# Kernel tuning notes

Hardware: AMD Instinct MI355X
Metric: run time of the kernel (lower is better)

Reference implementation:

```python
import jax, jax.numpy as jnp
import numpy as np

N_ITER = 50  # bisection iterations (matches entmax_bisect default)


def entmax_bisect(x, alpha):
    """alpha-entmax via bisection along axis=1. x: [B, L, 1], alpha: [1] (>1)."""
    a_m1 = alpha - 1.0
    inv = 1.0 / a_m1
    xs = x * a_m1
    d = x.shape[1]
    max_val = jnp.max(xs, axis=1, keepdims=True)
    tau_lo = max_val - 1.0
    tau_hi = max_val - (1.0 / d) ** a_m1
    f_lo = jnp.sum(jnp.maximum(xs - tau_lo, 0.0) ** inv, axis=1, keepdims=True) - 1.0

    def body(i, carry):
        tau_lo, dm = carry
        dm = dm * 0.5
        tau_m = tau_lo + dm
        f_m = jnp.sum(jnp.maximum(xs - tau_m, 0.0) ** inv, axis=1, keepdims=True) - 1.0
        tau_lo = jnp.where(f_m * f_lo >= 0.0, tau_m, tau_lo)
        return (tau_lo, dm)

    tau_lo, dm = jax.lax.fori_loop(0, N_ITER, body, (tau_lo, tau_hi - tau_lo))
    p = jnp.maximum(xs - (tau_lo + 0.5 * dm), 0.0) ** inv
    return p / jnp.sum(p, axis=1, keepdims=True)


def setup_inputs() -> dict:
    key = jax.random.key(0)
    ks = jax.random.split(key, 8)
    B, L, E2, D = 256, 512, 512, 256  # E2 = emb_size * 2
    C_target = jax.random.normal(ks[0], (B, E2), jnp.float32)
    C = jax.random.normal(ks[1], (B, L, E2), jnp.float32)
    X = jax.random.normal(ks[2], (B, E2, D), jnp.float32)
    alpha = jnp.array([1.5], jnp.float32)  # entmax-1.5
    mask = jax.random.randint(ks[3], (B, L), 0, 2, jnp.int32).at[:, 0].set(1)
    s = 1.0 / np.sqrt(E2)
    Wg1 = jax.random.uniform(ks[4], (E2, E2), jnp.float32, -s, s)
    Wg2 = jax.random.uniform(ks[5], (E2, E2), jnp.float32, -s, s)
    Wg0 = jax.random.uniform(ks[6], (E2, 1), jnp.float32, -s, s)
    bias_alpha = jax.random.normal(ks[7], (E2,), jnp.float32) * 0.02
    return dict(C_target=C_target, C=C, X=X, alpha=alpha, mask=mask,
                Wg1=Wg1, Wg2=Wg2, Wg0=Wg0, bias_alpha=bias_alpha)


def reference(C_target, C, X, alpha, mask, Wg1, Wg2, Wg0, bias_alpha):
    q = C_target[:, None, :]                               # [B, 1, 2E]
    h = jax.nn.relu(C @ Wg1 + q @ Wg2 + bias_alpha)        # [B, L, 2E]
    score = h @ Wg0                                        # [B, L, 1]
    score = jnp.where(mask[..., None] == 0, -1e30, score)  # mask -> -inf
    p = entmax_bisect(score, alpha)                        # sparse attn over L
    attn = jnp.swapaxes(p, 1, 2) @ C                       # [B, 1, 2E]
    out = jnp.sum(attn @ X, axis=1)                        # [B, D]
    return out
```

## Files before the change

kernel.cpp:

```cpp
#include <hip/hip_runtime.h>
#include <hip/hip_bf16.h>

typedef __bf16 bf16_t;
typedef bf16_t bf16x8 __attribute__((ext_vector_type(8)));
typedef float f32x4 __attribute__((ext_vector_type(4)));

__global__ void k_wg1t(const float* __restrict__ Wg1, bf16_t* __restrict__ Wg1T) {
    __shared__ float tile[32][33];
    const int k0 = blockIdx.x * 32;
    const int e0 = blockIdx.y * 32;
    const int tx = threadIdx.x;
    const int ty = threadIdx.y;
    #pragma unroll
    for (int i = 0; i < 32; i += 8)
        tile[ty + i][tx] = Wg1[(k0 + ty + i) * 512 + e0 + tx];
    __syncthreads();
    #pragma unroll
    for (int i = 0; i < 32; i += 8)
        Wg1T[(e0 + ty + i) * 512 + k0 + tx] = (bf16_t)tile[tx][ty + i];
}

__global__ __launch_bounds__(256) void k_gate(const float* __restrict__ Ct,
                                              const float* __restrict__ Wg2,
                                              const float* __restrict__ bias,
                                              float* __restrict__ g) {
    __shared__ float q[512];
    const int b = blockIdx.x;
    const int t = threadIdx.x;
    q[t]       = Ct[b * 512 + t];
    q[t + 256] = Ct[b * 512 + t + 256];
    __syncthreads();
    const int e = (blockIdx.y << 8) + t;
    float acc = bias[e];
    #pragma unroll 16
    for (int k = 0; k < 512; ++k)
        acc = fmaf(q[k], Wg2[k * 512 + e], acc);
    g[b * 512 + e] = acc;
}

__global__ __launch_bounds__(64) void k_compact(const int* __restrict__ mask,
                                                int* __restrict__ idx,
                                                int* __restrict__ nnz) {
    const int b    = blockIdx.x;
    const int lane = threadIdx.x;
    int base = 0;
    #pragma unroll
    for (int c = 0; c < 8; ++c) {
        const int l = (c << 6) + lane;
        const int v = mask[(b << 9) + l];
        const unsigned long long m = __ballot(v != 0);
        const int rank = __popcll(m & ((1ull << lane) - 1ull));
        if (v) idx[(b << 9) + base + rank] = l;
        base += __popcll(m);
    }
    if (lane == 0) nnz[b] = base;
}

__global__ __launch_bounds__(256, 2) void k_score(const float* __restrict__ C,
                                                  const bf16_t* __restrict__ Wg1T,
                                                  const float* __restrict__ g,
                                                  const float* __restrict__ Wg0,
                                                  const int* __restrict__ idx,
                                                  const int* __restrict__ nnz,
                                                  float* __restrict__ score) {
    __shared__ bf16_t As[64 * 512];
    __shared__ float  sred[4][64];
    __shared__ int    rs[64];

    const int t    = threadIdx.x;
    const int lane = t & 63;
    const int wave = t >> 6;
    const int quad = lane >> 4;
    const int l15  = lane & 15;

    const int bid  = blockIdx.x;
    const int b    = bid >> 3;
    const int tile = bid & 7;
    const int nb   = nnz[b];
    if (tile * 64 >= nb) return;

    if (t < 64) {
        const int j = tile * 64 + t;
        rs[t] = idx[(b << 9) + (j < nb ? j : nb - 1)];
    }
    __syncthreads();

    const float* Cb = C + ((size_t)b << 18);
    char* Asb = reinterpret_cast<char*>(As);
    #pragma unroll
    for (int i = 0; i < 32; ++i) {
        const int f = i * 256 + t;
        const int r = f >> 7;
        const int c = (f & 127) << 3;
        const float4 v = *reinterpret_cast<const float4*>(
            Cb + (size_t)rs[r] * 512 + ((f & 127) << 2));
        union { bf16_t h[4]; uint2 u; } pk;
        pk.h[0] = (bf16_t)v.x; pk.h[1] = (bf16_t)v.y;
        pk.h[2] = (bf16_t)v.z; pk.h[3] = (bf16_t)v.w;
        *reinterpret_cast<uint2*>(Asb + r * 1024 + (c ^ ((r & 7) << 4))) = pk.u;
    }
    __syncthreads();

    const bf16_t* bp[8];
    #pragma unroll
    for (int ni = 0; ni < 8; ++ni)
        bp[ni] = Wg1T + ((wave * 128 + ni * 16 + l15) << 9) + (quad << 3);

    const int swz = (l15 & 7) << 4;
    f32x4 acc[4][8] = {};
    #pragma unroll
    for (int kc = 0; kc < 16; ++kc) {
        bf16x8 afr[4], bfr[8];
        #pragma unroll
        for (int ni = 0; ni < 8; ++ni)
            bfr[ni] = *reinterpret_cast<const bf16x8*>(bp[ni] + (kc << 5));
        #pragma unroll
        for (int mi = 0; mi < 4; ++mi) {
            const int r  = mi * 16 + l15;
            const int cb = ((kc << 6) + (quad << 4)) ^ swz;
            afr[mi] = *reinterpret_cast<const bf16x8*>(
                reinterpret_cast<const char*>(As) + (r << 10) + cb);
        }
        #pragma unroll
        for (int mi = 0; mi < 4; ++mi)
            #pragma unroll
            for (int ni = 0; ni < 8; ++ni)
                acc[mi][ni] = __builtin_amdgcn_mfma_f32_16x16x32_bf16(
                    afr[mi], bfr[ni], acc[mi][ni], 0, 0, 0);
    }

    float rsum[16];
    #pragma unroll
    for (int i = 0; i < 16; ++i) rsum[i] = 0.f;
    #pragma unroll
    for (int ni = 0; ni < 8; ++ni) {
        const int n  = wave * 128 + ni * 16 + l15;
        const float gv = g[(b << 9) + n];
        const float w0 = Wg0[n];
        #pragma unroll
        for (int mi = 0; mi < 4; ++mi)
            #pragma unroll
            for (int r = 0; r < 4; ++r) {
                const float u = fmaxf(acc[mi][ni][r] + gv, 0.f);
                rsum[mi * 4 + r] = fmaf(u, w0, rsum[mi * 4 + r]);
            }
    }
    #pragma unroll
    for (int i = 0; i < 16; ++i) {
        float v = rsum[i];
        v += __shfl_xor(v, 1);
        v += __shfl_xor(v, 2);
        v += __shfl_xor(v, 4);
        v += __shfl_xor(v, 8);
        rsum[i] = v;
    }
    if (l15 == 0) {
        #pragma unroll
        for (int mi = 0; mi < 4; ++mi)
            #pragma unroll
            for (int r = 0; r < 4; ++r)
                sred[wave][mi * 16 + quad * 4 + r] = rsum[mi * 4 + r];
    }
    __syncthreads();
    if (t < 64 && tile * 64 + t < nb) {
        const float sc = sred[0][t] + sred[1][t] + sred[2][t] + sred[3][t];
        score[(b << 9) + rs[t]] = sc;
    }
}

__global__ __launch_bounds__(64) void k_entmax(const float* __restrict__ score,
                                               const int* __restrict__ mask,
                                               const float* __restrict__ alpha,
                                               int* __restrict__ sidx,
                                               float* __restrict__ sval,
                                               int* __restrict__ snnz) {
    const int lane = threadIdx.x;
    const int b    = blockIdx.x;
    const float am1 = alpha[0] - 1.0f;
    const float inv = 1.0f / am1;
    const bool  sq  = fabsf(inv - 2.0f) < 1e-6f;
    const float neg = -1e30f * am1;

    const float* sb = score + (b << 9);
    const int*   mb = mask  + (b << 9);
    float x[8];
    {
        const float4 v0 = *reinterpret_cast<const float4*>(sb + lane * 8);
        const float4 v1 = *reinterpret_cast<const float4*>(sb + lane * 8 + 4);
        const int4   m0 = *reinterpret_cast<const int4*>(mb + lane * 8);
        const int4   m1 = *reinterpret_cast<const int4*>(mb + lane * 8 + 4);
        x[0] = m0.x ? v0.x * am1 : neg; x[1] = m0.y ? v0.y * am1 : neg;
        x[2] = m0.z ? v0.z * am1 : neg; x[3] = m0.w ? v0.w * am1 : neg;
        x[4] = m1.x ? v1.x * am1 : neg; x[5] = m1.y ? v1.y * am1 : neg;
        x[6] = m1.z ? v1.z * am1 : neg; x[7] = m1.w ? v1.w * am1 : neg;
    }
    float m = x[0];
    #pragma unroll
    for (int j = 1; j < 8; ++j) m = fmaxf(m, x[j]);
    #pragma unroll
    for (int s = 1; s < 64; s <<= 1) m = fmaxf(m, __shfl_xor(m, s));

    float tau_lo = m - 1.0f;
    float dm = (m - powf(1.0f / 512.0f, am1)) - tau_lo;

    float f_lo;
    {
        float s = 0.f;
        #pragma unroll
        for (int j = 0; j < 8; ++j) {
            const float u = fmaxf(x[j] - tau_lo, 0.f);
            s += sq ? u * u : powf(u, inv);
        }
        #pragma unroll
        for (int sh = 1; sh < 64; sh <<= 1) s += __shfl_xor(s, sh);
        f_lo = s - 1.0f;
    }
    for (int it = 0; it < 50; ++it) {
        dm *= 0.5f;
        const float tau_m = tau_lo + dm;
        float s = 0.f;
        #pragma unroll
        for (int j = 0; j < 8; ++j) {
            const float u = fmaxf(x[j] - tau_m, 0.f);
            s += sq ? u * u : powf(u, inv);
        }
        #pragma unroll
        for (int sh = 1; sh < 64; sh <<= 1) s += __shfl_xor(s, sh);
        if ((s - 1.0f) * f_lo >= 0.f) tau_lo = tau_m;
    }
    const float tau = tau_lo + 0.5f * dm;
    float pj[8];
    float Z = 0.f;
    #pragma unroll
    for (int j = 0; j < 8; ++j) {
        const float u = fmaxf(x[j] - tau, 0.f);
        pj[j] = sq ? u * u : powf(u, inv);
        Z += pj[j];
    }
    #pragma unroll
    for (int sh = 1; sh < 64; sh <<= 1) Z += __shfl_xor(Z, sh);
    const float rz = 1.0f / Z;

    int base = 0;
    #pragma unroll
    for (int j = 0; j < 8; ++j) {
        const float pv = pj[j] * rz;
        const unsigned long long bm = __ballot(pv > 0.f);
        const int rank = __popcll(bm & ((1ull << lane) - 1ull));
        if (pv > 0.f) {
            sidx[(b << 9) + base + rank] = lane * 8 + j;
            sval[(b << 9) + base + rank] = pv;
        }
        base += __popcll(bm);
    }
    if (lane == 0) snnz[b] = base;
}

__global__ __launch_bounds__(256) void k_attn(const int* __restrict__ sidx,
                                              const float* __restrict__ sval,
                                              const int* __restrict__ snnz,
                                              const float* __restrict__ C,
                                              float* __restrict__ attn) {
    __shared__ int   li[128];
    __shared__ float lv[128];
    const int b  = blockIdx.x;
    const int ch = blockIdx.y;
    const int t  = threadIdx.x;
    const int n  = snnz[b];
    const int j0 = ch << 7;
    if (j0 >= n) return;
    const int cnt = min(n - j0, 128);
    if (t < cnt) {
        li[t] = sidx[(b << 9) + j0 + t];
        lv[t] = sval[(b << 9) + j0 + t];
    }
    __syncthreads();
    const float* Cb = C + ((size_t)b << 18);
    float a0 = 0.f, a1 = 0.f;
    int j = 0;
    for (; j + 8 <= cnt; j += 8) {
        #pragma unroll
        for (int u = 0; u < 8; ++u) {
            const float  w  = lv[j + u];
            const float* cr = Cb + ((size_t)li[j + u] << 9);
            a0 = fmaf(w, cr[t], a0);
            a1 = fmaf(w, cr[t + 256], a1);
        }
    }
    for (; j < cnt; ++j) {
        const float  w  = lv[j];
        const float* cr = Cb + ((size_t)li[j] << 9);
        a0 = fmaf(w, cr[t], a0);
        a1 = fmaf(w, cr[t + 256], a1);
    }
    atomicAdd(&attn[(b << 9) + t], a0);
    atomicAdd(&attn[(b << 9) + t + 256], a1);
}

__global__ __launch_bounds__(256) void k_out(const float* __restrict__ attn,
                                             const float* __restrict__ X,
                                             float* __restrict__ out) {
    __shared__ float as_[256];
    __shared__ f32x4 red[4][64];
    const int b    = blockIdx.x;
    const int ec   = blockIdx.y;
    const int t    = threadIdx.x;
    const int wave = t >> 6;
    const int lane = t & 63;
    as_[t] = attn[(b << 9) + (ec << 8) + t];
    __syncthreads();
    const float4* Xb = reinterpret_cast<const float4*>(
        X + ((size_t)b << 17) + ((size_t)ec << 16));
    f32x4 a = {};
    #pragma unroll 8
    for (int e = wave; e < 256; e += 4) {
        const float  w = as_[e];
        const float4 v = Xb[e * 64 + lane];
        a[0] = fmaf(w, v.x, a[0]);
        a[1] = fmaf(w, v.y, a[1]);
        a[2] = fmaf(w, v.z, a[2]);
        a[3] = fmaf(w, v.w, a[3]);
    }
    red[wave][lane] = a;
    __syncthreads();
    if (wave == 0) {
        const f32x4 s = red[0][lane] + red[1][lane] + red[2][lane] + red[3][lane];
        #pragma unroll
        for (int r = 0; r < 4; ++r)
            atomicAdd(&out[(b << 8) + lane * 4 + r], s[r]);
    }
}

extern "C" void kernel_launch(void* const* d_in, const int* in_sizes, int n_in,
                              void* d_out, int out_size, void* d_ws, size_t ws_size,
                              hipStream_t stream) {
    const float* C_target = (const float*)d_in[0];
    const float* C        = (const float*)d_in[1];
    const float* X        = (const float*)d_in[2];
    const float* alpha    = (const float*)d_in[3];
    const int*   mask     = (const int*)  d_in[4];
    const float* Wg1      = (const float*)d_in[5];
    const float* Wg2      = (const float*)d_in[6];
    const float* Wg0      = (const float*)d_in[7];
    const float* bias     = (const float*)d_in[8];
    float* out = (float*)d_out;

    char* ws = (char*)d_ws;
    bf16_t* wg1t  = (bf16_t*)(ws);
    float*  g     = (float*)(ws + ( 512u << 10));
    float*  score = (float*)(ws + (1024u << 10));
    int*    idx   = (int*)  (ws + (1536u << 10));
    int*    sidx  = (int*)  (ws + (2048u << 10));
    float*  sval  = (float*)(ws + (2560u << 10));
    float*  attn  = (float*)(ws + (3072u << 10));
    int*    nnz   = (int*)  (ws + (3584u << 10));
    int*    snnz  = (int*)  (ws + (3584u << 10) + 4096);

    k_wg1t   <<<dim3(16, 16), dim3(32, 8), 0, stream>>>(Wg1, wg1t);
    k_gate   <<<dim3(256, 2), 256, 0, stream>>>(C_target, Wg2, bias, g);
    k_compact<<<256, 64, 0, stream>>>(mask, idx, nnz);
    k_score  <<<2048, 256, 0, stream>>>(C, wg1t, g, Wg0, idx, nnz, score);
    k_entmax <<<256, 64, 0, stream>>>(score, mask, alpha, sidx, sval, snnz);
    hipMemsetAsync(attn, 0, 512u << 10, stream);
    k_attn   <<<dim3(256, 4), 256, 0, stream>>>(sidx, sval, snnz, C, attn);
    hipMemsetAsync(d_out, 0, (size_t)out_size * sizeof(float), stream);
    k_out    <<<dim3(256, 2), 256, 0, stream>>>(attn, X, out);
}
```

Baseline: 619.4 us.

## Fuse prep and post kernels, rework score GEMM to direct global A loads

Merges transpose, gate GEMV and mask compaction into one launch, and fuses entmax, the attention gather and the X projection into a single per-batch kernel. This removes the intermediate buffers, both memsets and the atomics. The score kernel drops the LDS staging of C and loads A rows straight from global memory into MFMA fragments, using 32-row tiles and a higher occupancy target. The trade-offs are less A reuse through LDS and fewer blocks for the post stage, which now runs only 256 blocks.

Result: slower. 786.6 us (+27.0%).

```diff
diff --git a/kernel.cpp b/kernel.cpp
--- a/kernel.cpp
+++ b/kernel.cpp
@@ -5,67 +5,70 @@
 typedef bf16_t bf16x8 __attribute__((ext_vector_type(8)));
 typedef float f32x4 __attribute__((ext_vector_type(4)));
 
-__global__ void k_wg1t(const float* __restrict__ Wg1, bf16_t* __restrict__ Wg1T) {
-    __shared__ float tile[32][33];
-    const int k0 = blockIdx.x * 32;
-    const int e0 = blockIdx.y * 32;
-    const int tx = threadIdx.x;
-    const int ty = threadIdx.y;
-    #pragma unroll
-    for (int i = 0; i < 32; i += 8)
-        tile[ty + i][tx] = Wg1[(k0 + ty + i) * 512 + e0 + tx];
-    __syncthreads();
-    #pragma unroll
-    for (int i = 0; i < 32; i += 8)
-        Wg1T[(e0 + ty + i) * 512 + k0 + tx] = (bf16_t)tile[tx][ty + i];
-}
-
-__global__ __launch_bounds__(256) void k_gate(const float* __restrict__ Ct,
+__global__ __launch_bounds__(256) void k_prep(const float* __restrict__ Wg1,
+                                              bf16_t* __restrict__ Wg1T,
+                                              const float* __restrict__ Ct,
                                               const float* __restrict__ Wg2,
                                               const float* __restrict__ bias,
-                                              float* __restrict__ g) {
-    __shared__ float q[512];
-    const int b = blockIdx.x;
-    const int t = threadIdx.x;
-    q[t]       = Ct[b * 512 + t];
-    q[t + 256] = Ct[b * 512 + t + 256];
-    __syncthreads();
-    const int e = (blockIdx.y << 8) + t;
-    float acc = bias[e];
-    #pragma unroll 16
-    for (int k = 0; k < 512; ++k)
-        acc = fmaf(q[k], Wg2[k * 512 + e], acc);
-    g[b * 512 + e] = acc;
+                                              float* __restrict__ g,
+                                              const int* __restrict__ mask,
+                                              int* __restrict__ idx,
+                                              int* __restrict__ nnz) {
+    const int bid = blockIdx.x;
+    const int t   = threadIdx.x;
+    if (bid < 256) {
+        __shared__ float tile[32][33];
+        const int k0 = (bid & 15) << 5;
+        const int e0 = (bid >> 4) << 5;
+        const int tx = t & 31;
+        const int ty = t >> 5;
+        #pragma unroll
+        for (int i = 0; i < 32; i += 8)
+            tile[ty + i][tx] = Wg1[(k0 + ty + i) * 512 + e0 + tx];
+        __syncthreads();
+        #pragma unroll
+        for (int i = 0; i < 32; i += 8)
+            Wg1T[(e0 + ty + i) * 512 + k0 + tx] = (bf16_t)tile[tx][ty + i];
+    } else if (bid < 768) {
+        __shared__ float q[512];
+        const int gb = bid - 256;
+        const int b  = gb >> 1;
+        q[t]       = Ct[b * 512 + t];
+        q[t + 256] = Ct[b * 512 + t + 256];
+        __syncthreads();
+        const int e = ((gb & 1) << 8) + t;
+        float acc = bias[e];
+        #pragma unroll 16
+        for (int k = 0; k < 512; ++k)
+            acc = fmaf(q[k], Wg2[k * 512 + e], acc);
+        g[b * 512 + e] = acc;
+    } else {
+        const int b = bid - 768;
+        if (t < 64) {
+            const int lane = t;
+            int base = 0;
+            #pragma unroll
+            for (int c = 0; c < 8; ++c) {
+                const int l = (c << 6) + lane;
+                const int v = mask[(b << 9) + l];
+                const unsigned long long m = __ballot(v != 0);
+                const int rank = __popcll(m & ((1ull << lane) - 1ull));
+                if (v) idx[(b << 9) + base + rank] = l;
+                base += __popcll(m);
+            }
+            if (lane == 0) nnz[b] = base;
+        }
+    }
 }
 
-__global__ __launch_bounds__(64) void k_compact(const int* __restrict__ mask,
-                                                int* __restrict__ idx,
-                                                int* __restrict__ nnz) {
-    const int b    = blockIdx.x;
-    const int lane = threadIdx.x;
-    int base = 0;
-    #pragma unroll
-    for (int c = 0; c < 8; ++c) {
-        const int l = (c << 6) + lane;
-        const int v = mask[(b << 9) + l];
-        const unsigned long long m = __ballot(v != 0);
-        const int rank = __popcll(m & ((1ull << lane) - 1ull));
-        if (v) idx[(b << 9) + base + rank] = l;
-        base += __popcll(m);
-    }
-    if (lane == 0) nnz[b] = base;
-}
-
-__global__ __launch_bounds__(256, 2) void k_score(const float* __restrict__ C,
+__global__ __launch_bounds__(256, 3) void k_score(const float* __restrict__ C,
                                                   const bf16_t* __restrict__ Wg1T,
                                                   const float* __restrict__ g,
                                                   const float* __restrict__ Wg0,
                                                   const int* __restrict__ idx,
                                                   const int* __restrict__ nnz,
                                                   float* __restrict__ score) {
-    __shared__ bf16_t As[64 * 512];
-    __shared__ float  sred[4][64];
-    __shared__ int    rs[64];
+    __shared__ float sred[4][32];
 
     const int t    = threadIdx.x;
     const int lane = t & 63;
@@ -74,71 +77,74 @@
     const int l15  = lane & 15;
 
     const int bid  = blockIdx.x;
-    const int b    = bid >> 3;
-    const int tile = bid & 7;
+    const int b    = bid >> 4;
+    const int tile = bid & 15;
     const int nb   = nnz[b];
-    if (tile * 64 >= nb) return;
-
-    if (t < 64) {
-        const int j = tile * 64 + t;
-        rs[t] = idx[(b << 9) + (j < nb ? j : nb - 1)];
-    }
-    __syncthreads();
-
-    const float* Cb = C + ((size_t)b << 18);
-    char* Asb = reinterpret_cast<char*>(As);
+    if (tile * 32 >= nb) return;
+
+    const int j0  = tile * 32 + l15;
+    const int j1  = j0 + 16;
+    const int rs0 = idx[(b << 9) + (j0 < nb ? j0 : nb - 1)];
+    const int rs1 = idx[(b << 9) + (j1 < nb ? j1 : nb - 1)];
+
+    const float* Cb  = C + ((size_t)b << 18);
+    const float* Ab0 = Cb + (size_t)rs0 * 512 + (quad << 3);
+    const float* Ab1 = Cb + (size_t)rs1 * 512 + (quad << 3);
+    const bf16_t* Bb = Wg1T + (((wave << 7) + l15) << 9) + (quad << 3);
+
+    f32x4 acc[2][8] = {};
+
+    #pragma unroll 2
+    for (int kc = 0; kc < 16; ++kc) {
+        const float4 a00 = *reinterpret_cast<const float4*>(Ab0 + (kc << 5));
+        const float4 a01 = *reinterpret_cast<const float4*>(Ab0 + (kc << 5) + 4);
+        const float4 a10 = *reinterpret_cast<const float4*>(Ab1 + (kc << 5));
+        const float4 a11 = *reinterpret_cast<const float4*>(Ab1 + (kc << 5) + 4);
+        union { bf16_t h[8]; bf16x8 v; } ua0, ua1;
+        ua0.h[0] = (bf16_t)a00.x; ua0.h[1] = (bf16_t)a00.y;
+        ua0.h[2] = (bf16_t)a00.z; ua0.h[3] = (bf16_t)a00.w;
+        ua0.h[4] = (bf16_t)a01.x; ua0.h[5] = (bf16_t)a01.y;
+        ua0.h[6] = (bf16_t)a01.z; ua0.h[7] = (bf16_t)a01.w;
+        ua1.h[0] = (bf16_t)a10.x; ua1.h[1] = (bf16_t)a10.y;
+        ua1.h[2] = (bf16_t)a10.z; ua1.h[3] = (bf16_t)a10.w;
+        ua1.h[4] = (bf16_t)a11.x; ua1.h[5] = (bf16_t)a11.y;
+        ua1.h[6] = (bf16_t)a11.z; ua1.h[7] = (bf16_t)a11.w;
+
+        bf16x8 bfr[4];
+        #pragma unroll
+        for (int ni = 0; ni < 4; ++ni)
+            bfr[ni] = *reinterpret_cast<const bf16x8*>(
+                Bb + ((size_t)ni << 13) + (kc << 5));
+        #pragma unroll
+        for (int ni = 0; ni < 4; ++ni) {
+            acc[0][ni] = __builtin_amdgcn_mfma_f32_16x16x32_bf16(
+                ua0.v, bfr[ni], acc[0][ni], 0, 0, 0);
+            acc[1][ni] = __builtin_amdgcn_mfma_f32_16x16x32_bf16(
+                ua1.v, bfr[ni], acc[1][ni], 0, 0, 0);
+        }
+        #pragma unroll
+        for (int ni = 0; ni < 4; ++ni)
+            bfr[ni] = *reinterpret_cast<const bf16x8*>(
+                Bb + ((size_t)(ni + 4) << 13) + (kc << 5));
+        #pragma unroll
+        for (int ni = 0; ni < 4; ++ni) {
+            acc[0][ni + 4] = __builtin_amdgcn_mfma_f32_16x16x32_bf16(
+                ua0.v, bfr[ni], acc[0][ni + 4], 0, 0, 0);
+            acc[1][ni + 4] = __builtin_amdgcn_mfma_f32_16x16x32_bf16(
+                ua1.v, bfr[ni], acc[1][ni + 4], 0, 0, 0);
+        }
+    }
+
+    float rsum[8];
     #pragma unroll
-    for (int i = 0; i < 32; ++i) {
-        const int f = i * 256 + t;
-        const int r = f >> 7;
-        const int c = (f & 127) << 3;
-        const float4 v = *reinterpret_cast<const float4*>(
-            Cb + (size_t)rs[r] * 512 + ((f & 127) << 2));
-        union { bf16_t h[4]; uint2 u; } pk;
-        pk.h[0] = (bf16_t)v.x; pk.h[1] = (bf16_t)v.y;
-        pk.h[2] = (bf16_t)v.z; pk.h[3] = (bf16_t)v.w;
-        *reinterpret_cast<uint2*>(Asb + r * 1024 + (c ^ ((r & 7) << 4))) = pk.u;
-    }
-    __syncthreads();
-
-    const bf16_t* bp[8];
-    #pragma unroll
-    for (int ni = 0; ni < 8; ++ni)
-        bp[ni] = Wg1T + ((wave * 128 + ni * 16 + l15) << 9) + (quad << 3);
-
-    const int swz = (l15 & 7) << 4;
-    f32x4 acc[4][8] = {};
-    #pragma unroll
-    for (int kc = 0; kc < 16; ++kc) {
-        bf16x8 afr[4], bfr[8];
-        #pragma unroll
-        for (int ni = 0; ni < 8; ++ni)
-            bfr[ni] = *reinterpret_cast<const bf16x8*>(bp[ni] + (kc << 5));
-        #pragma unroll
-        for (int mi = 0; mi < 4; ++mi) {
-            const int r  = mi * 16 + l15;
-            const int cb = ((kc << 6) + (quad << 4)) ^ swz;
-            afr[mi] = *reinterpret_cast<const bf16x8*>(
-                reinterpret_cast<const char*>(As) + (r << 10) + cb);
-        }
-        #pragma unroll
-        for (int mi = 0; mi < 4; ++mi)
-            #pragma unroll
-            for (int ni = 0; ni < 8; ++ni)
-                acc[mi][ni] = __builtin_amdgcn_mfma_f32_16x16x32_bf16(
-                    afr[mi], bfr[ni], acc[mi][ni], 0, 0, 0);
-    }
-
-    float rsum[16];
-    #pragma unroll
-    for (int i = 0; i < 16; ++i) rsum[i] = 0.f;
+    for (int i = 0; i < 8; ++i) rsum[i] = 0.f;
     #pragma unroll
     for (int ni = 0; ni < 8; ++ni) {
-        const int n  = wave * 128 + ni * 16 + l15;
+        const int n  = (wave << 7) + (ni << 4) + l15;
         const float gv = g[(b << 9) + n];
         const float w0 = Wg0[n];
         #pragma unroll
-        for (int mi = 0; mi < 4; ++mi)
+        for (int mi = 0; mi < 2; ++mi)
             #pragma unroll
             for (int r = 0; r < 4; ++r) {
                 const float u = fmaxf(acc[mi][ni][r] + gv, 0.f);
@@ -146,7 +152,7 @@
             }
     }
     #pragma unroll
-    for (int i = 0; i < 16; ++i) {
+    for (int i = 0; i < 8; ++i) {
         float v = rsum[i];
         v += __shfl_xor(v, 1);
         v += __shfl_xor(v, 2);
@@ -156,178 +162,162 @@
     }
     if (l15 == 0) {
         #pragma unroll
-        for (int mi = 0; mi < 4; ++mi)
+        for (int mi = 0; mi < 2; ++mi)
             #pragma unroll
             for (int r = 0; r < 4; ++r)
                 sred[wave][mi * 16 + quad * 4 + r] = rsum[mi * 4 + r];
     }
     __syncthreads();
-    if (t < 64 && tile * 64 + t < nb) {
-        const float sc = sred[0][t] + sred[1][t] + sred[2][t] + sred[3][t];
-        score[(b << 9) + rs[t]] = sc;
+    if (t < 32) {
+        const int j = tile * 32 + t;
+        if (j < nb) {
+            const float sc = sred[0][t] + sred[1][t] + sred[2][t] + sred[3][t];
+            score[(b << 9) + idx[(b << 9) + j]] = sc;
+        }
     }
 }
 
-__global__ __launch_bounds__(64) void k_entmax(const float* __restrict__ score,
-                                               const int* __restrict__ mask,
-                                               const float* __restrict__ alpha,
-                                               int* __restrict__ sidx,
-                                               float* __restrict__ sval,
-                                               int* __restrict__ snnz) {
-    const int lane = threadIdx.x;
-    const int b    = blockIdx.x;
-    const float am1 = alpha[0] - 1.0f;
-    const float inv = 1.0f / am1;
-    const bool  sq  = fabsf(inv - 2.0f) < 1e-6f;
-    const float neg = -1e30f * am1;
-
-    const float* sb = score + (b << 9);
-    const int*   mb = mask  + (b << 9);
-    float x[8];
-    {
-        const float4 v0 = *reinterpret_cast<const float4*>(sb + lane * 8);
-        const float4 v1 = *reinterpret_cast<const float4*>(sb + lane * 8 + 4);
-        const int4   m0 = *reinterpret_cast<const int4*>(mb + lane * 8);
-        const int4   m1 = *reinterpret_cast<const int4*>(mb + lane * 8 + 4);
-        x[0] = m0.x ? v0.x * am1 : neg; x[1] = m0.y ? v0.y * am1 : neg;
-        x[2] = m0.z ? v0.z * am1 : neg; x[3] = m0.w ? v0.w * am1 : neg;
-        x[4] = m1.x ? v1.x * am1 : neg; x[5] = m1.y ? v1.y * am1 : neg;
-        x[6] = m1.z ? v1.z * am1 : neg; x[7] = m1.w ? v1.w * am1 : neg;
-    }
-    float m = x[0];
-    #pragma unroll
-    for (int j = 1; j < 8; ++j) m = fmaxf(m, x[j]);
-    #pragma unroll
-    for (int s = 1; s < 64; s <<= 1) m = fmaxf(m, __shfl_xor(m, s));
-
-    float tau_lo = m - 1.0f;
-    float dm = (m - powf(1.0f / 512.0f, am1)) - tau_lo;
-
-    float f_lo;
-    {
-        float s = 0.f;
+__global__ __launch_bounds__(256) void k_post(const float* __restrict__ score,
+                                              const int* __restrict__ mask,
+                                              const float* __restrict__ alpha,
+                                              const float* __restrict__ C,
+                                              const float* __restrict__ X,
+                                              float* __restrict__ out) {
+    __shared__ float sup_v[512];
+    __shared__ int   sup_i[512];
+    __shared__ int   s_n;
+    __shared__ float attn_s[512];
+    __shared__ f32x4 red[4][64];
+
+    const int b = blockIdx.x;
+    const int t = threadIdx.x;
+
+    if (t < 64) {
+        const int lane = t;
+        const float am1 = alpha[0] - 1.0f;
+        const float inv = 1.0f / am1;
+        const bool  sq  = fabsf(inv - 2.0f) < 1e-6f;
+        const float neg = -1e30f * am1;
+
+        const float* sb = score + (b << 9);
+        const int*   mb = mask  + (b << 9);
+        float x[8];
+        {
+            const float4 v0 = *reinterpret_cast<const float4*>(sb + lane * 8);
+            const float4 v1 = *reinterpret_cast<const float4*>(sb + lane * 8 + 4);
+            const int4   m0 = *reinterpret_cast<const int4*>(mb + lane * 8);
+            const int4   m1 = *reinterpret_cast<const int4*>(mb + lane * 8 + 4);
+            x[0] = m0.x ? v0.x * am1 : neg; x[1] = m0.y ? v0.y * am1 : neg;
+            x[2] = m0.z ? v0.z * am1 : neg; x[3] = m0.w ? v0.w * am1 : neg;
+            x[4] = m1.x ? v1.x * am1 : neg; x[5] = m1.y ? v1.y * am1 : neg;
+            x[6] = m1.z ? v1.z * am1 : neg; x[7] = m1.w ? v1.w * am1 : neg;
+        }
+        float m = x[0];
+        #pragma unroll
+        for (int j = 1; j < 8; ++j) m = fmaxf(m, x[j]);
+        #pragma unroll
+        for (int s = 1; s < 64; s <<= 1) m = fmaxf(m, __shfl_xor(m, s));
+
+        float tau_lo = m - 1.0f;
+        float dm = (m - powf(1.0f / 512.0f, am1)) - tau_lo;
+
+        float f_lo;
+        {
+            float s = 0.f;
+            #pragma unroll
+            for (int j = 0; j < 8; ++j) {
+                const float u = fmaxf(x[j] - tau_lo, 0.f);
+                s += sq ? u * u : powf(u, inv);
+            }
+            #pragma unroll
+            for (int sh = 1; sh < 64; sh <<= 1) s += __shfl_xor(s, sh);
+            f_lo = s - 1.0f;
+        }
+        for (int it = 0; it < 50; ++it) {
+            dm *= 0.5f;
+            const float tau_m = tau_lo + dm;
+            float s = 0.f;
+            #pragma unroll
+            for (int j = 0; j < 8; ++j) {
+                const float u = fmaxf(x[j] - tau_m, 0.f);
+                s += sq ? u * u : powf(u, inv);
+            }
+            #pragma unroll
+            for (int sh = 1; sh < 64; sh <<= 1) s += __shfl_xor(s, sh);
+            if ((s - 1.0f) * f_lo >= 0.f) tau_lo = tau_m;
+        }
+        const float tau = tau_lo + 0.5f * dm;
+        float pj[8];
+        float Z = 0.f;
         #pragma unroll
         for (int j = 0; j < 8; ++j) {
-            const float u = fmaxf(x[j] - tau_lo, 0.f);
-            s += sq ? u * u : powf(u, inv);
-        }
-        #pragma unroll
-        for (int sh = 1; sh < 64; sh <<= 1) s += __shfl_xor(s, sh);
-        f_lo = s - 1.0f;
-    }
-    for (int it = 0; it < 50; ++it) {
-        dm *= 0.5f;
-        const float tau_m = tau_lo + dm;
-        float s = 0.f;
+            const float u = fmaxf(x[j] - tau, 0.f);
+            pj[j] = sq ? u * u : powf(u, inv);
+            Z += pj[j];
+        }
+        #pragma unroll
+        for (int sh = 1; sh < 64; sh <<= 1) Z += __shfl_xor(Z, sh);
+        const float rz = 1.0f / Z;
+
+        int base = 0;
         #pragma unroll
         for (int j = 0; j < 8; ++j) {
-            const float u = fmaxf(x[j] - tau_m, 0.f);
-            s += sq ? u * u : powf(u, inv);
-        }
-        #pragma unroll
-        for (int sh = 1; sh < 64; sh <<= 1) s += __shfl_xor(s, sh);
-        if ((s - 1.0f) * f_lo >= 0.f) tau_lo = tau_m;
-    }
-    const float tau = tau_lo + 0.5f * dm;
-    float pj[8];
-    float Z = 0.f;
-    #pragma unroll
-    for (int j = 0; j < 8; ++j) {
-        const float u = fmaxf(x[j] - tau, 0.f);
-        pj[j] = sq ? u * u : powf(u, inv);
-        Z += pj[j];
-    }
-    #pragma unroll
-    for (int sh = 1; sh < 64; sh <<= 1) Z += __shfl_xor(Z, sh);
-    const float rz = 1.0f / Z;
-
-    int base = 0;
-    #pragma unroll
-    for (int j = 0; j < 8; ++j) {
-        const float pv = pj[j] * rz;
-        const unsigned long long bm = __ballot(pv > 0.f);
-        const int rank = __popcll(bm & ((1ull << lane) - 1ull));
-        if (pv > 0.f) {
-            sidx[(b << 9) + base + rank] = lane * 8 + j;
-            sval[(b << 9) + base + rank] = pv;
-        }
-        base += __popcll(bm);
-    }
-    if (lane == 0) snnz[b] = base;
-}
-
-__global__ __launch_bounds__(256) void k_attn(const int* __restrict__ sidx,
-                                              const float* __restrict__ sval,
-                                              const int* __restrict__ snnz,
-                                              const float* __restrict__ C,
-                                              float* __restrict__ attn) {
-    __shared__ int   li[128];
-    __shared__ float lv[128];
-    const int b  = blockIdx.x;
-    const int ch = blockIdx.y;
-    const int t  = threadIdx.x;
-    const int n  = snnz[b];
-    const int j0 = ch << 7;
-    if (j0 >= n) return;
-    const int cnt = min(n - j0, 128);
-    if (t < cnt) {
-        li[t] = sidx[(b << 9) + j0 + t];
-        lv[t] = sval[(b << 9) + j0 + t];
+            const float pv = pj[j] * rz;
+            const unsigned long long bm = __ballot(pv > 0.f);
+            const int rank = __popcll(bm & ((1ull << lane) - 1ull));
+            if (pv > 0.f) {
+                sup_i[base + rank] = lane * 8 + j;
+                sup_v[base + rank] = pv;
+            }
+            base += __popcll(bm);
+        }
+        if (lane == 0) s_n = base;
     }
     __syncthreads();
+
+    const int n = s_n;
     const float* Cb = C + ((size_t)b << 18);
     float a0 = 0.f, a1 = 0.f;
     int j = 0;
-    for (; j + 8 <= cnt; j += 8) {
-        #pragma unroll
-        for (int u = 0; u < 8; ++u) {
-            const float  w  = lv[j + u];
-            const float* cr = Cb + ((size_t)li[j + u] << 9);
+    for (; j + 4 <= n; j += 4) {
+        #pragma unroll
+        for (int u = 0; u < 4; ++u) {
+            const float  w  = sup_v[j + u];
+            const float* cr = Cb + ((size_t)sup_i[j + u] << 9);
             a0 = fmaf(w, cr[t], a0);
             a1 = fmaf(w, cr[t + 256], a1);
         }
     }
-    for (; j < cnt; ++j) {
-        const float  w  = lv[j];
-        const float* cr = Cb + ((size_t)li[j] << 9);
+    for (; j < n; ++j) {
+        const float  w  = sup_v[j];
+        const float* cr = Cb + ((size_t)sup_i[j] << 9);
         a0 = fmaf(w, cr[t], a0);
         a1 = fmaf(w, cr[t + 256], a1);
     }
-    atomicAdd(&attn[(b << 9) + t], a0);
-    atomicAdd(&attn[(b << 9) + t + 256], a1);
-}
-
-__global__ __launch_bounds__(256) void k_out(const float* __restrict__ attn,
-                                             const float* __restrict__ X,
-                                             float* __restrict__ out) {
-    __shared__ float as_[256];
-    __shared__ f32x4 red[4][64];
-    const int b    = blockIdx.x;
-    const int ec   = blockIdx.y;
-    const int t    = threadIdx.x;
-    const int wave = t >> 6;
-    const int lane = t & 63;
-    as_[t] = attn[(b << 9) + (ec << 8) + t];
+    attn_s[t]       = a0;
+    attn_s[t + 256] = a1;
     __syncthreads();
-    const float4* Xb = reinterpret_cast<const float4*>(
-        X + ((size_t)b << 17) + ((size_t)ec << 16));
+
+    const int eg = t >> 6;
+    const int d4 = t & 63;
+    const float4* Xb = reinterpret_cast<const float4*>(X + ((size_t)b << 17));
     f32x4 a = {};
     #pragma unroll 8
-    for (int e = wave; e < 256; e += 4) {
-        const float  w = as_[e];
-        const float4 v = Xb[e * 64 + lane];
+    for (int e = eg; e < 512; e += 4) {
+        const float  w = attn_s[e];
+        const float4 v = Xb[e * 64 + d4];
         a[0] = fmaf(w, v.x, a[0]);
         a[1] = fmaf(w, v.y, a[1]);
         a[2] = fmaf(w, v.z, a[2]);
         a[3] = fmaf(w, v.w, a[3]);
     }
-    red[wave][lane] = a;
+    red[eg][d4] = a;
     __syncthreads();
-    if (wave == 0) {
-        const f32x4 s = red[0][lane] + red[1][lane] + red[2][lane] + red[3][lane];
-        #pragma unroll
-        for (int r = 0; r < 4; ++r)
-            atomicAdd(&out[(b << 8) + lane * 4 + r], s[r]);
+    if (t < 64) {
+        const f32x4 s = red[0][t] + red[1][t] + red[2][t] + red[3][t];
+        float4 o;
+        o.x = s[0]; o.y = s[1]; o.z = s[2]; o.w = s[3];
+        *reinterpret_cast<float4*>(out + (b << 8) + (t << 2)) = o;
     }
 }
 
@@ -350,19 +340,10 @@
     float*  g     = (float*)(ws + ( 512u << 10));
     float*  score = (float*)(ws + (1024u << 10));
     int*    idx   = (int*)  (ws + (1536u << 10));
-    int*    sidx  = (int*)  (ws + (2048u << 10));
-    float*  sval  = (float*)(ws + (2560u << 10));
-    float*  attn  = (float*)(ws + (3072u << 10));
-    int*    nnz   = (int*)  (ws + (3584u << 10));
-    int*    snnz  = (int*)  (ws + (3584u << 10) + 4096);
-
-    k_wg1t   <<<dim3(16, 16), dim3(32, 8), 0, stream>>>(Wg1, wg1t);
-    k_gate   <<<dim3(256, 2), 256, 0, stream>>>(C_target, Wg2, bias, g);
-    k_compact<<<256, 64, 0, stream>>>(mask, idx, nnz);
-    k_score  <<<2048, 256, 0, stream>>>(C, wg1t, g, Wg0, idx, nnz, score);
-    k_entmax <<<256, 64, 0, stream>>>(score, mask, alpha, sidx, sval, snnz);
-    hipMemsetAsync(attn, 0, 512u << 10, stream);
-    k_attn   <<<dim3(256, 4), 256, 0, stream>>>(sidx, sval, snnz, C, attn);
-    hipMemsetAsync(d_out, 0, (size_t)out_size * sizeof(float), stream);
-    k_out    <<<dim3(256, 2), 256, 0, stream>>>(attn, X, out);
+    int*    nnz   = (int*)  (ws + (2048u << 10));
+
+    k_prep  <<<1024, 256, 0, stream>>>(Wg1, wg1t, C_target, Wg2, bias, g,
+                                       mask, idx, nnz);
+    k_score <<<4096, 256, 0, stream>>>(C, wg1t, g, Wg0, idx, nnz, score);
+    k_post  <<<256, 256, 0, stream>>>(score, mask, alpha, C, X, out);
 }
```
